# Performance work log

Measured on AMD Instinct MI355X. Metric: run time of the kernel, lower is better.

## Reference

```python
import jax, jax.numpy as jnp
import numpy as np

B, N1, N2, DIM1, DIM2, DK = 4, 4096, 2048, 256, 256, 256


def setup_inputs() -> dict:
    key = jax.random.key(0)
    ks = jax.random.split(key, 8)
    s1 = 1.0 / np.sqrt(DIM2)  # torch Linear default init scale (uniform bound)
    s2 = 1.0 / np.sqrt(DIM1)
    return {
        "x1": jax.random.normal(ks[0], (B, N1, DIM1), jnp.float32),
        "x2": jax.random.normal(ks[1], (B, N2, DIM2), jnp.float32),
        "WQ": jax.random.uniform(ks[2], (DK, DIM2), jnp.float32, -s1, s1),
        "bQ": jax.random.uniform(ks[3], (DK,), jnp.float32, -s1, s1),
        "WK": jax.random.uniform(ks[4], (DK, DIM1), jnp.float32, -s2, s2),
        "bK": jax.random.uniform(ks[5], (DK,), jnp.float32, -s2, s2),
        "WV": jax.random.uniform(ks[6], (DK, DIM1), jnp.float32, -s2, s2),
        "bV": jax.random.uniform(ks[7], (DK,), jnp.float32, -s2, s2),
    }


def reference(x1, x2, WQ, bQ, WK, bK, WV, bV):
    # Projections (torch Linear: x @ W^T + b)
    Q = jnp.einsum('bnd,kd->bnk', x2, WQ) + bQ  # [B, N2, DK]
    K = jnp.einsum('bmd,kd->bmk', x1, WK) + bK  # [B, N1, DK]
    V = jnp.einsum('bmd,kd->bmk', x1, WV) + bV  # [B, N1, DK]

    QK = jnp.einsum('bnk,bmk->bnm', Q, K)                          # [B, N2, N1]
    P = (jnp.einsum('bnk,bmk->bnm', jnp.tanh(Q), jnp.tanh(K)) + 1.0) * 0.5
    scores = QK * P / jnp.sqrt(jnp.float32(DK))
    attn = jax.nn.softmax(scores, axis=-1)                         # [B, N2, N1]
    Q_hat = jnp.einsum('bnm,bmk->bnk', attn, V)                    # [B, N2, DK]
    return (Q, Q_hat, attn)
```

## Files before the change

kernel.cpp:

```cpp
#include <hip/hip_runtime.h>
#include <hip/hip_bf16.h>

typedef __bf16 bf16;
typedef __bf16 bf16x4 __attribute__((ext_vector_type(4)));
typedef __bf16 bf16x8 __attribute__((ext_vector_type(8)));
typedef float  f32x4  __attribute__((ext_vector_type(4)));

#define DEVI static __device__ __forceinline__

constexpr int NB = 4;
constexpr int N1 = 4096;
constexpr int N2 = 2048;
constexpr int D  = 256;

DEVI f32x4 mfma16(bf16x8 a, bf16x8 b, f32x4 c) {
  return __builtin_amdgcn_mfma_f32_16x16x32_bf16(a, b, c, 0, 0, 0);
}

typedef const __attribute__((address_space(1))) void* gas_t;
typedef __attribute__((address_space(3))) void* las_t;

DEVI void gload_lds16(const void* g, void* l) {
  __builtin_amdgcn_global_load_lds((gas_t)g, (las_t)l, 16, 0, 0);
}

DEVI void fence_sched() { __builtin_amdgcn_sched_barrier(0); }

DEVI void projQ_body(bf16* smem,
                     const float* __restrict__ A, const float* __restrict__ Bm,
                     const float* __restrict__ bias,
                     float* __restrict__ outF, bf16* __restrict__ out1,
                     bf16* __restrict__ out2, int bx, int by)
{
  bf16* Ah = smem;
  bf16* Al = smem + 8192;
  bf16* Bh = smem + 16384;
  bf16* Bl = smem + 20480;
  const int tid  = threadIdx.x;
  const int lane = tid & 63, wid = tid >> 6;
  const int wr = wid >> 1, wc = wid & 1;
  const int m0 = bx * 128, n0 = by * 64;

  f32x4 acc[4][2];
#pragma unroll
  for (int i = 0; i < 4; ++i)
#pragma unroll
    for (int j = 0; j < 2; ++j) acc[i][j] = f32x4{0.f, 0.f, 0.f, 0.f};

  for (int kt = 0; kt < 4; ++kt) {
    const int k0 = kt * 64;
    if (kt) __syncthreads();
#pragma unroll
    for (int i = 0; i < 8; ++i) {
      int idx = i * 256 + tid;
      int r = idx >> 4, c4 = idx & 15;
      const float4 v = *(const float4*)(A + (size_t)(m0 + r) * D + k0 + c4 * 4);
      bf16x4 h, l;
      h[0] = (bf16)v.x; h[1] = (bf16)v.y; h[2] = (bf16)v.z; h[3] = (bf16)v.w;
      l[0] = (bf16)(v.x - (float)h[0]); l[1] = (bf16)(v.y - (float)h[1]);
      l[2] = (bf16)(v.z - (float)h[2]); l[3] = (bf16)(v.w - (float)h[3]);
      *(bf16x4*)&Ah[r * 64 + c4 * 4] = h;
      *(bf16x4*)&Al[r * 64 + c4 * 4] = l;
    }
#pragma unroll
    for (int i = 0; i < 4; ++i) {
      int idx = i * 256 + tid;
      int r = idx >> 4, c4 = idx & 15;
      const float4 v = *(const float4*)(Bm + (size_t)(n0 + r) * D + k0 + c4 * 4);
      bf16x4 h, l;
      h[0] = (bf16)v.x; h[1] = (bf16)v.y; h[2] = (bf16)v.z; h[3] = (bf16)v.w;
      l[0] = (bf16)(v.x - (float)h[0]); l[1] = (bf16)(v.y - (float)h[1]);
      l[2] = (bf16)(v.z - (float)h[2]); l[3] = (bf16)(v.w - (float)h[3]);
      *(bf16x4*)&Bh[r * 64 + c4 * 4] = h;
      *(bf16x4*)&Bl[r * 64 + c4 * 4] = l;
    }
    __syncthreads();
#pragma unroll
    for (int kc = 0; kc < 2; ++kc) {
      const int ko = kc * 32 + (lane >> 4) * 8;
      bf16x8 ah[4], al[4];
#pragma unroll
      for (int mf = 0; mf < 4; ++mf) {
        ah[mf] = *(bf16x8*)&Ah[(wr * 64 + mf * 16 + (lane & 15)) * 64 + ko];
        al[mf] = *(bf16x8*)&Al[(wr * 64 + mf * 16 + (lane & 15)) * 64 + ko];
      }
#pragma unroll
      for (int nf = 0; nf < 2; ++nf) {
        bf16x8 bh = *(bf16x8*)&Bh[(wc * 32 + nf * 16 + (lane & 15)) * 64 + ko];
        bf16x8 bl = *(bf16x8*)&Bl[(wc * 32 + nf * 16 + (lane & 15)) * 64 + ko];
#pragma unroll
        for (int mf = 0; mf < 4; ++mf) {
          acc[mf][nf] = mfma16(ah[mf], bh, acc[mf][nf]);
          acc[mf][nf] = mfma16(ah[mf], bl, acc[mf][nf]);
          acc[mf][nf] = mfma16(al[mf], bh, acc[mf][nf]);
        }
      }
    }
  }

#pragma unroll
  for (int nf = 0; nf < 2; ++nf) {
    const int col = n0 + wc * 32 + nf * 16 + (lane & 15);
    const float bcol = bias[col];
#pragma unroll
    for (int mf = 0; mf < 4; ++mf) {
#pragma unroll
      for (int r = 0; r < 4; ++r) {
        const int row = m0 + wr * 64 + mf * 16 + (lane >> 4) * 4 + r;
        float v = acc[mf][nf][r] + bcol;
        outF[(size_t)row * D + col] = v;
        out1[(size_t)row * D + col] = (bf16)v;
        out2[(size_t)row * D + col] = (bf16)tanhf(v);
      }
    }
  }
}

template<int MODE>
DEVI void proj_body(bf16* smem,
                    const float* __restrict__ A, const float* __restrict__ Bm,
                    const float* __restrict__ bias,
                    bf16* __restrict__ out1, bf16* __restrict__ out2,
                    int bx, int by)
{
  bf16* As = smem;
  bf16* Bs = smem + 8192;
  const int tid  = threadIdx.x;
  const int lane = tid & 63, wid = tid >> 6;
  const int wr = wid >> 1, wc = wid & 1;
  const int m0 = bx * 128, n0 = by * 64;

  f32x4 acc[4][2];
#pragma unroll
  for (int i = 0; i < 4; ++i)
#pragma unroll
    for (int j = 0; j < 2; ++j) acc[i][j] = f32x4{0.f, 0.f, 0.f, 0.f};

  for (int kt = 0; kt < 4; ++kt) {
    const int k0 = kt * 64;
    if (kt) __syncthreads();
#pragma unroll
    for (int i = 0; i < 8; ++i) {
      int idx = i * 256 + tid;
      int r = idx >> 4, c4 = idx & 15;
      const float4 v = *(const float4*)(A + (size_t)(m0 + r) * D + k0 + c4 * 4);
      bf16x4 bv; bv[0] = (bf16)v.x; bv[1] = (bf16)v.y; bv[2] = (bf16)v.z; bv[3] = (bf16)v.w;
      *(bf16x4*)&As[r * 64 + c4 * 4] = bv;
    }
#pragma unroll
    for (int i = 0; i < 4; ++i) {
      int idx = i * 256 + tid;
      int r = idx >> 4, c4 = idx & 15;
      const float4 v = *(const float4*)(Bm + (size_t)(n0 + r) * D + k0 + c4 * 4);
      bf16x4 bv; bv[0] = (bf16)v.x; bv[1] = (bf16)v.y; bv[2] = (bf16)v.z; bv[3] = (bf16)v.w;
      *(bf16x4*)&Bs[r * 64 + c4 * 4] = bv;
    }
    __syncthreads();
#pragma unroll
    for (int kc = 0; kc < 2; ++kc) {
      const int ko = kc * 32 + (lane >> 4) * 8;
      bf16x8 a[4];
#pragma unroll
      for (int mf = 0; mf < 4; ++mf)
        a[mf] = *(bf16x8*)&As[(wr * 64 + mf * 16 + (lane & 15)) * 64 + ko];
#pragma unroll
      for (int nf = 0; nf < 2; ++nf) {
        bf16x8 bb = *(bf16x8*)&Bs[(wc * 32 + nf * 16 + (lane & 15)) * 64 + ko];
#pragma unroll
        for (int mf = 0; mf < 4; ++mf) acc[mf][nf] = mfma16(a[mf], bb, acc[mf][nf]);
      }
    }
  }

#pragma unroll
  for (int nf = 0; nf < 2; ++nf) {
    const int col = n0 + wc * 32 + nf * 16 + (lane & 15);
    float bcol = 0.f;
    if constexpr (MODE == 1) bcol = bias[col];
#pragma unroll
    for (int mf = 0; mf < 4; ++mf) {
#pragma unroll
      for (int r = 0; r < 4; ++r) {
        const int row = m0 + wr * 64 + mf * 16 + (lane >> 4) * 4 + r;
        float v = acc[mf][nf][r];
        if constexpr (MODE == 1) {
          v += bcol;
          out1[(size_t)row * D + col] = (bf16)v;
          out2[(size_t)row * D + col] = (bf16)tanhf(v);
        } else {
          v += bias[row];
          out1[(size_t)(col >> 12) * (D * N1) + (size_t)row * N1 + (col & 4095)] = (bf16)v;
        }
      }
    }
  }
}

__global__ __launch_bounds__(256)
void proj_all_kernel(const float* __restrict__ x1, const float* __restrict__ x2,
                     const float* __restrict__ WQ, const float* __restrict__ bQ,
                     const float* __restrict__ WK, const float* __restrict__ bK,
                     const float* __restrict__ WV, const float* __restrict__ bV,
                     float* __restrict__ Qf, bf16* __restrict__ Qb,
                     bf16* __restrict__ tQb, bf16* __restrict__ Kb,
                     bf16* __restrict__ tKb, bf16* __restrict__ Vt)
{
  __shared__ bf16 smem[24576];
  const int bid = blockIdx.x;
  if (bid < 512) {
    proj_body<1>(smem, x1, WK, bK, Kb, tKb, bid & 127, bid >> 7);
  } else if (bid < 768) {
    const int b2 = bid - 512;
    projQ_body(smem, x2, WQ, bQ, Qf, Qb, tQb, b2 & 63, b2 >> 6);
  } else {
    const int b3 = bid - 768;
    proj_body<2>(smem, WV, x1, bV, Vt, nullptr, b3 & 1, b3 >> 1);
  }
}

__global__ __launch_bounds__(256, 2)
void scores_kernel(const bf16* __restrict__ Qb, const bf16* __restrict__ tQb,
                   const bf16* __restrict__ Kb, const bf16* __restrict__ tKb,
                   bf16* __restrict__ E, float* __restrict__ partials)
{
  __shared__ bf16 SM[2][4][128][32];
  __shared__ float rowpart[128][2];
  const int tid = threadIdx.x, lane = tid & 63, wid = tid >> 6;
  const int wr = wid >> 1;
  const int wc = wid & 1;
  const int lo16 = lane & 15, hi = lane >> 4;
  const int mt = blockIdx.x, nt = blockIdx.y, b = blockIdx.z;
  const int RQ = b * N2 + nt * 128;
  const int RK = b * N1 + mt * 128;

  f32x4 accS[4][4], accP[4][4];
#pragma unroll
  for (int i = 0; i < 4; ++i)
#pragma unroll
    for (int j = 0; j < 4; ++j) {
      accS[i][j] = f32x4{0.f, 0.f, 0.f, 0.f};
      accP[i][j] = f32x4{0.f, 0.f, 0.f, 0.f};
    }

  auto stage = [&](int kt, int buf) {
#pragma unroll
    for (int i = 0; i < 2; ++i) {
      const int c = i * 256 + tid;
      const int row = c >> 2;
      const int soff = kt * 32 + (((c & 3) ^ ((row >> 1) & 3)) << 3);
      char* dst = (char*)&SM[buf][0][0][0] + c * 16;
      gload_lds16(Qb  + (size_t)(RQ + row) * D + soff, dst);
      gload_lds16(tQb + (size_t)(RQ + row) * D + soff, dst + 8192);
      gload_lds16(Kb  + (size_t)(RK + row) * D + soff, dst + 16384);
      gload_lds16(tKb + (size_t)(RK + row) * D + soff, dst + 24576);
    }
  };

  auto cpt = [&](int buf) {
    bf16x8 aS[4], aT[4];
#pragma unroll
    for (int mf = 0; mf < 4; ++mf) {
      const int row = wr * 64 + mf * 16 + lo16;
      const int ko = (hi ^ ((row >> 1) & 3)) << 3;
      aS[mf] = *(bf16x8*)&SM[buf][0][row][ko];
      aT[mf] = *(bf16x8*)&SM[buf][1][row][ko];
    }
#pragma unroll
    for (int nf = 0; nf < 4; ++nf) {
      const int row = wc * 64 + nf * 16 + lo16;
      const int ko = (hi ^ ((row >> 1) & 3)) << 3;
      bf16x8 bS = *(bf16x8*)&SM[buf][2][row][ko];
      bf16x8 bT = *(bf16x8*)&SM[buf][3][row][ko];
#pragma unroll
      for (int mf = 0; mf < 4; ++mf) {
        accS[mf][nf] = mfma16(aS[mf], bS, accS[mf][nf]);
        accP[mf][nf] = mfma16(aT[mf], bT, accP[mf][nf]);
      }
    }
  };

  stage(0, 0);
  fence_sched();
  int cur = 0;
#pragma unroll
  for (int kt = 0; kt < 8; ++kt) {
    if (kt < 7) {
      stage(kt + 1, cur ^ 1);
      fence_sched();
      asm volatile("s_waitcnt vmcnt(8)\n\ts_barrier" ::: "memory");
    } else {
      asm volatile("s_waitcnt vmcnt(0)\n\ts_barrier" ::: "memory");
    }
    __builtin_amdgcn_s_setprio(1);
    cpt(cur);
    __builtin_amdgcn_s_setprio(0);
    asm volatile("s_barrier" ::: "memory");
    cur ^= 1;
  }

#pragma unroll
  for (int mf = 0; mf < 4; ++mf) {
    f32x4 rs = f32x4{0.f, 0.f, 0.f, 0.f};
#pragma unroll
    for (int nf = 0; nf < 4; ++nf) {
      const int m_g = mt * 128 + wc * 64 + nf * 16 + lo16;
#pragma unroll
      for (int r = 0; r < 4; ++r) {
        const int n_g = b * N2 + nt * 128 + wr * 64 + mf * 16 + hi * 4 + r;
        float s = accS[mf][nf][r] * (accP[mf][nf][r] + 1.0f) * 0.03125f;
        float e = __expf(s);
        E[(size_t)n_g * N1 + m_g] = (bf16)e;
        rs[r] += e;
      }
    }
#pragma unroll
    for (int r = 0; r < 4; ++r) {
      float v = rs[r];
      v += __shfl_xor(v, 1); v += __shfl_xor(v, 2);
      v += __shfl_xor(v, 4); v += __shfl_xor(v, 8);
      if (lo16 == 0)
        rowpart[wr * 64 + mf * 16 + hi * 4 + r][wc] = v;
    }
  }
  __syncthreads();
  if (tid < 128) {
    float p = rowpart[tid][0] + rowpart[tid][1];
    partials[(size_t)(b * N2 + nt * 128 + tid) * 32 + mt] = p;
  }
}

__global__ __launch_bounds__(512)
void qhat_kernel(const bf16* __restrict__ E, const bf16* __restrict__ Vt,
                 const float* __restrict__ partials,
                 float* __restrict__ attn, bf16* __restrict__ partQ)
{
  __shared__ bf16 Es[2][128][64];
  __shared__ bf16 Vs[2][256][64];
  __shared__ float rowinv[128];
  const int tid = threadIdx.x, lane = tid & 63, wid = tid >> 6;
  const int lo16 = lane & 15, hi = lane >> 4;
  const int wr = wid & 3;
  const int wh = wid >> 2;
  const int wgid = blockIdx.x;
  const int xcd  = wgid & 7;
  const int slot = wgid >> 3;
  const int combo = xcd * 2 + (slot >> 4);
  const int nt = slot & 15;
  const int q  = combo >> 2;
  const int b  = combo & 3;
  const int n0 = nt * 128;
  const int mq = q * 1024;
  const size_t nbase = (size_t)b * N2 + n0;
  const bf16* vb = Vt + (size_t)b * (D * N1) + mq;

  if (tid < 128) {
    const float* pr = partials + (nbase + tid) * 32;
    f32x4 s4 = *(const f32x4*)pr;
#pragma unroll
    for (int j = 1; j < 8; ++j) s4 += *(const f32x4*)(pr + j * 4);
    rowinv[tid] = 1.0f / (s4[0] + s4[1] + s4[2] + s4[3]);
  }

  auto stage = [&](int ms, int buf) {
#pragma unroll
    for (int i = 0; i < 2; ++i) {
      const int c = i * 512 + tid;
      const int row = c >> 3;
      const int lg = (c & 7) ^ (row & 7);
      gload_lds16(E + (nbase + row) * N1 + mq + ms * 64 + lg * 8,
                  (char*)&Es[buf][0][0] + c * 16);
    }
#pragma unroll
    for (int i = 0; i < 4; ++i) {
      const int c = i * 512 + tid;
      const int row = c >> 3;
      const int lg = (c & 7) ^ (row & 7);
      gload_lds16(vb + (size_t)row * N1 + ms * 64 + lg * 8,
                  (char*)&Vs[buf][0][0] + c * 16);
    }
  };

  f32x4 acc[2][8];
#pragma unroll
  for (int i = 0; i < 2; ++i)
#pragma unroll
    for (int j = 0; j < 8; ++j) acc[i][j] = f32x4{0.f, 0.f, 0.f, 0.f};

  auto cpt = [&](int buf) {
#pragma unroll
    for (int kc = 0; kc < 2; ++kc) {
      bf16x8 a[2];
#pragma unroll
      for (int mf = 0; mf < 2; ++mf) {
        const int row = wr * 32 + mf * 16 + lo16;
        const int ph = (kc * 4 + hi) ^ (row & 7);
        a[mf] = *(bf16x8*)((char*)&Es[buf][0][0] + row * 128 + ph * 16);
      }
#pragma unroll
      for (int nf = 0; nf < 8; ++nf) {
        const int row = wh * 128 + nf * 16 + lo16;
        const int ph = (kc * 4 + hi) ^ (row & 7);
        bf16x8 bb = *(bf16x8*)((char*)&Vs[buf][0][0] + row * 128 + ph * 16);
        acc[0][nf] = mfma16(a[0], bb, acc[0][nf]);
        acc[1][nf] = mfma16(a[1], bb, acc[1][nf]);
      }
    }
  };

  auto attnwrite = [&](int ms, int buf) {
#pragma unroll
    for (int i = 0; i < 2; ++i) {
      const int c = i * 512 + tid;
      const int row = c >> 3;
      const int lg = (c & 7) ^ (row & 7);
      bf16x8 ev = *(bf16x8*)((char*)&Es[buf][0][0] + c * 16);
      const float inv = rowinv[row];
      float v[8];
#pragma unroll
      for (int j = 0; j < 8; ++j) v[j] = (float)ev[j] * inv;
      float* dst = attn + (nbase + row) * N1 + mq + ms * 64 + lg * 8;
      float4 w0 = {v[0], v[1], v[2], v[3]};
      float4 w1 = {v[4], v[5], v[6], v[7]};
      *(float4*)(dst)     = w0;
      *(float4*)(dst + 4) = w1;
    }
  };

  stage(0, 0);
  fence_sched();
  __syncthreads();

  int buf = 0;
  for (int ms = 0; ms < 16; ++ms) {
    if (ms < 15) { stage(ms + 1, buf ^ 1); fence_sched(); }
    if (ms == 0)
      asm volatile("s_waitcnt vmcnt(6)\n\ts_barrier" ::: "memory");
    else if (ms < 15)
      asm volatile("s_waitcnt vmcnt(10)\n\ts_barrier" ::: "memory");
    else
      asm volatile("s_waitcnt vmcnt(4)\n\ts_barrier" ::: "memory");
    __builtin_amdgcn_s_setprio(1);
    cpt(buf);
    __builtin_amdgcn_s_setprio(0);
    attnwrite(ms, buf);
    asm volatile("s_barrier" ::: "memory");
    buf ^= 1;
  }

#pragma unroll
  for (int mf = 0; mf < 2; ++mf)
#pragma unroll
    for (int nf = 0; nf < 8; ++nf)
#pragma unroll
      for (int r = 0; r < 4; ++r) {
        const int n  = n0 + wr * 32 + mf * 16 + hi * 4 + r;
        const int dk = wh * 128 + nf * 16 + lo16;
        partQ[((size_t)(q * NB + b) * N2 + n) * D + dk] = (bf16)acc[mf][nf][r];
      }
}

__global__ __launch_bounds__(256)
void reduceQ_kernel(const bf16* __restrict__ P, const float* __restrict__ partials,
                    float* __restrict__ Qhat)
{
  const int tid = threadIdx.x;
  const size_t rn = (size_t)blockIdx.x * 8 + (tid >> 5);
  const int j = tid & 31;
  float s = partials[rn * 32 + j];
  s += __shfl_xor(s, 1); s += __shfl_xor(s, 2); s += __shfl_xor(s, 4);
  s += __shfl_xor(s, 8); s += __shfl_xor(s, 16);
  const float inv = 1.0f / s;

  const size_t base = rn * 256 + (size_t)j * 8;
  const size_t S = (size_t)NB * N2 * D;
  bf16x8 p0 = *(const bf16x8*)(P + base);
  bf16x8 p1 = *(const bf16x8*)(P + S + base);
  bf16x8 p2 = *(const bf16x8*)(P + 2 * S + base);
  bf16x8 p3 = *(const bf16x8*)(P + 3 * S + base);
  float o[8];
#pragma unroll
  for (int jj = 0; jj < 8; ++jj)
    o[jj] = (((float)p0[jj] + (float)p1[jj]) + ((float)p2[jj] + (float)p3[jj])) * inv;
  float4 w0 = {o[0], o[1], o[2], o[3]};
  float4 w1 = {o[4], o[5], o[6], o[7]};
  *(float4*)(Qhat + base)     = w0;
  *(float4*)(Qhat + base + 4) = w1;
}

extern "C" void kernel_launch(void* const* d_in, const int* in_sizes, int n_in,
                              void* d_out, int out_size, void* d_ws, size_t ws_size,
                              hipStream_t stream)
{
  const float* x1 = (const float*)d_in[0];
  const float* x2 = (const float*)d_in[1];
  const float* WQ = (const float*)d_in[2];
  const float* bQ = (const float*)d_in[3];
  const float* WK = (const float*)d_in[4];
  const float* bK = (const float*)d_in[5];
  const float* WV = (const float*)d_in[6];
  const float* bV = (const float*)d_in[7];

  float* out  = (float*)d_out;
  float* Qf   = out;
  float* Qhat = out + 2097152;
  float* attn = out + 4194304;

  char* ws = (char*)d_ws;
  bf16* Qb   = (bf16*)(ws + (0ull  << 20));
  bf16* tQb  = (bf16*)(ws + (4ull  << 20));
  bf16* Kb   = (bf16*)(ws + (8ull  << 20));
  bf16* tKb  = (bf16*)(ws + (16ull << 20));
  bf16* Vt   = (bf16*)(ws + (24ull << 20));
  bf16* E    = (bf16*)(ws + (32ull << 20));
  float* partials = (float*)(ws + (96ull << 20));
  bf16*  partQ    = (bf16*)(ws + (100ull << 20));

  proj_all_kernel <<<1280, 256, 0, stream>>>(x1, x2, WQ, bQ, WK, bK, WV, bV,
                                             Qf, Qb, tQb, Kb, tKb, Vt);
  scores_kernel   <<<dim3(32, 16, 4), 256, 0, stream>>>(Qb, tQb, Kb, tKb, E, partials);
  qhat_kernel     <<<256, 512, 0, stream>>>(E, Vt, partials, attn, partQ);
  reduceQ_kernel  <<<1024, 256, 0, stream>>>(partQ, partials, Qhat);
}
```

Before: 147.6 us.

## Widen scores tile to 128x256 with 8 waves and triple-buffered K-loop

The scores kernel now computes a 128x256 output tile per block using 512 threads (8 waves in a 2x4 grid), so each staged Q tile is reused across twice as many K rows. This halves the number of blocks and the Q reload traffic. The K-loop moves from double to triple buffering with a prefetch distance of two and adjusted vmcnt waits, to hide more global-load latency. Per-row partial sums drop from 32 to 16 entries, and the downstream qhat and reduce kernels are updated to match. Shared memory per block grows and occupancy falls to one large block per CU.

```diff
diff --git a/kernel.cpp b/kernel.cpp
--- a/kernel.cpp
+++ b/kernel.cpp
@@ -218,20 +218,21 @@
   }
 }
 
-__global__ __launch_bounds__(256, 2)
+__global__ __launch_bounds__(512, 1)
 void scores_kernel(const bf16* __restrict__ Qb, const bf16* __restrict__ tQb,
                    const bf16* __restrict__ Kb, const bf16* __restrict__ tKb,
                    bf16* __restrict__ E, float* __restrict__ partials)
 {
-  __shared__ bf16 SM[2][4][128][32];
-  __shared__ float rowpart[128][2];
+  __shared__ bf16 SMQ[3][2][128][32];
+  __shared__ bf16 SMK[3][2][256][32];
+  __shared__ float rowpart[128][4];
   const int tid = threadIdx.x, lane = tid & 63, wid = tid >> 6;
-  const int wr = wid >> 1;
-  const int wc = wid & 1;
+  const int wr = wid >> 2;
+  const int wc = wid & 3;
   const int lo16 = lane & 15, hi = lane >> 4;
   const int mt = blockIdx.x, nt = blockIdx.y, b = blockIdx.z;
   const int RQ = b * N2 + nt * 128;
-  const int RK = b * N1 + mt * 128;
+  const int RK = b * N1 + mt * 256;
 
   f32x4 accS[4][4], accP[4][4];
 #pragma unroll
@@ -242,17 +243,24 @@
       accP[i][j] = f32x4{0.f, 0.f, 0.f, 0.f};
     }
 
+  const int qrow = tid >> 2;
+  const int qsc  = (((tid & 3) ^ ((qrow >> 1) & 3)) << 3);
+
   auto stage = [&](int kt, int buf) {
+    const int k0 = kt * 32;
+    gload_lds16(Qb  + (size_t)(RQ + qrow) * D + k0 + qsc,
+                (char*)&SMQ[buf][0][0][0] + tid * 16);
+    gload_lds16(tQb + (size_t)(RQ + qrow) * D + k0 + qsc,
+                (char*)&SMQ[buf][1][0][0] + tid * 16);
 #pragma unroll
     for (int i = 0; i < 2; ++i) {
-      const int c = i * 256 + tid;
+      const int c = i * 512 + tid;
       const int row = c >> 2;
-      const int soff = kt * 32 + (((c & 3) ^ ((row >> 1) & 3)) << 3);
-      char* dst = (char*)&SM[buf][0][0][0] + c * 16;
-      gload_lds16(Qb  + (size_t)(RQ + row) * D + soff, dst);
-      gload_lds16(tQb + (size_t)(RQ + row) * D + soff, dst + 8192);
-      gload_lds16(Kb  + (size_t)(RK + row) * D + soff, dst + 16384);
-      gload_lds16(tKb + (size_t)(RK + row) * D + soff, dst + 24576);
+      const int sc = (((c & 3) ^ ((row >> 1) & 3)) << 3);
+      gload_lds16(Kb  + (size_t)(RK + row) * D + k0 + sc,
+                  (char*)&SMK[buf][0][0][0] + c * 16);
+      gload_lds16(tKb + (size_t)(RK + row) * D + k0 + sc,
+                  (char*)&SMK[buf][1][0][0] + c * 16);
     }
   };
 
@@ -262,15 +270,15 @@
     for (int mf = 0; mf < 4; ++mf) {
       const int row = wr * 64 + mf * 16 + lo16;
       const int ko = (hi ^ ((row >> 1) & 3)) << 3;
-      aS[mf] = *(bf16x8*)&SM[buf][0][row][ko];
-      aT[mf] = *(bf16x8*)&SM[buf][1][row][ko];
+      aS[mf] = *(bf16x8*)&SMQ[buf][0][row][ko];
+      aT[mf] = *(bf16x8*)&SMQ[buf][1][row][ko];
     }
 #pragma unroll
     for (int nf = 0; nf < 4; ++nf) {
       const int row = wc * 64 + nf * 16 + lo16;
       const int ko = (hi ^ ((row >> 1) & 3)) << 3;
-      bf16x8 bS = *(bf16x8*)&SM[buf][2][row][ko];
-      bf16x8 bT = *(bf16x8*)&SM[buf][3][row][ko];
+      bf16x8 bS = *(bf16x8*)&SMK[buf][0][row][ko];
+      bf16x8 bT = *(bf16x8*)&SMK[buf][1][row][ko];
 #pragma unroll
       for (int mf = 0; mf < 4; ++mf) {
         accS[mf][nf] = mfma16(aS[mf], bS, accS[mf][nf]);
@@ -281,21 +289,26 @@
 
   stage(0, 0);
   fence_sched();
-  int cur = 0;
+  stage(1, 1);
+  fence_sched();
 #pragma unroll
   for (int kt = 0; kt < 8; ++kt) {
-    if (kt < 7) {
-      stage(kt + 1, cur ^ 1);
+    const int buf = kt - (kt / 3) * 3;
+    if (kt < 6) {
+      const int nb = (kt + 2) - ((kt + 2) / 3) * 3;
+      stage(kt + 2, nb);
       fence_sched();
-      asm volatile("s_waitcnt vmcnt(8)\n\ts_barrier" ::: "memory");
-    } else {
+    }
+    if (kt < 6)
+      asm volatile("s_waitcnt vmcnt(12)\n\ts_barrier" ::: "memory");
+    else if (kt == 6)
+      asm volatile("s_waitcnt vmcnt(6)\n\ts_barrier" ::: "memory");
+    else
       asm volatile("s_waitcnt vmcnt(0)\n\ts_barrier" ::: "memory");
-    }
     __builtin_amdgcn_s_setprio(1);
-    cpt(cur);
+    cpt(buf);
     __builtin_amdgcn_s_setprio(0);
     asm volatile("s_barrier" ::: "memory");
-    cur ^= 1;
   }
 
 #pragma unroll
@@ -303,7 +316,7 @@
     f32x4 rs = f32x4{0.f, 0.f, 0.f, 0.f};
 #pragma unroll
     for (int nf = 0; nf < 4; ++nf) {
-      const int m_g = mt * 128 + wc * 64 + nf * 16 + lo16;
+      const int m_g = mt * 256 + wc * 64 + nf * 16 + lo16;
 #pragma unroll
       for (int r = 0; r < 4; ++r) {
         const int n_g = b * N2 + nt * 128 + wr * 64 + mf * 16 + hi * 4 + r;
@@ -324,8 +337,8 @@
   }
   __syncthreads();
   if (tid < 128) {
-    float p = rowpart[tid][0] + rowpart[tid][1];
-    partials[(size_t)(b * N2 + nt * 128 + tid) * 32 + mt] = p;
+    float p = rowpart[tid][0] + rowpart[tid][1] + rowpart[tid][2] + rowpart[tid][3];
+    partials[(size_t)(b * N2 + nt * 128 + tid) * 16 + mt] = p;
   }
 }
 
@@ -354,10 +367,10 @@
   const bf16* vb = Vt + (size_t)b * (D * N1) + mq;
 
   if (tid < 128) {
-    const float* pr = partials + (nbase + tid) * 32;
+    const float* pr = partials + (nbase + tid) * 16;
     f32x4 s4 = *(const f32x4*)pr;
 #pragma unroll
-    for (int j = 1; j < 8; ++j) s4 += *(const f32x4*)(pr + j * 4);
+    for (int j = 1; j < 4; ++j) s4 += *(const f32x4*)(pr + j * 4);
     rowinv[tid] = 1.0f / (s4[0] + s4[1] + s4[2] + s4[3]);
   }
 
@@ -466,9 +479,9 @@
   const int tid = threadIdx.x;
   const size_t rn = (size_t)blockIdx.x * 8 + (tid >> 5);
   const int j = tid & 31;
-  float s = partials[rn * 32 + j];
+  float s = partials[rn * 16 + (j & 15)];
   s += __shfl_xor(s, 1); s += __shfl_xor(s, 2); s += __shfl_xor(s, 4);
-  s += __shfl_xor(s, 8); s += __shfl_xor(s, 16);
+  s += __shfl_xor(s, 8);
   const float inv = 1.0f / s;
 
   const size_t base = rn * 256 + (size_t)j * 8;
@@ -517,7 +530,7 @@
 
   proj_all_kernel <<<1280, 256, 0, stream>>>(x1, x2, WQ, bQ, WK, bK, WV, bV,
                                              Qf, Qb, tQb, Kb, tKb, Vt);
-  scores_kernel   <<<dim3(32, 16, 4), 256, 0, stream>>>(Qb, tQb, Kb, tKb, E, partials);
+  scores_kernel   <<<dim3(16, 16, 4), 512, 0, stream>>>(Qb, tQb, Kb, tKb, E, partials);
   qhat_kernel     <<<256, 512, 0, stream>>>(E, Vt, partials, attn, partQ);
   reduceQ_kernel  <<<1024, 256, 0, stream>>>(partQ, partials, Qhat);
 }
```

New measurement: 149.3 us. Within noise of the previous version (+1.1%).

## Fuse Q-hat split reduction into qhat kernel via last-block atomic counter

Applied to the files above, without the earlier changes.

Removes the separate reduceQ kernel launch. Each qhat workgroup now atomically increments a per-(batch,row-tile) counter after writing its partial Q-hat, and the last of the four split-M workgroups sums the partials and normalizes them using the already-loaded row inverse. The counters are zeroed in the projection kernel. This saves a launch and a pass over the partials, but the reduction tail now runs serially inside the last-arriving workgroups and adds fences and atomics.

```diff
diff --git a/kernel.cpp b/kernel.cpp
--- a/kernel.cpp
+++ b/kernel.cpp
@@ -203,10 +203,12 @@
                      const float* __restrict__ WV, const float* __restrict__ bV,
                      float* __restrict__ Qf, bf16* __restrict__ Qb,
                      bf16* __restrict__ tQb, bf16* __restrict__ Kb,
-                     bf16* __restrict__ tKb, bf16* __restrict__ Vt)
+                     bf16* __restrict__ tKb, bf16* __restrict__ Vt,
+                     int* __restrict__ qcnt)
 {
   __shared__ bf16 smem[24576];
   const int bid = blockIdx.x;
+  if (bid == 0 && threadIdx.x < 64) qcnt[threadIdx.x] = 0;
   if (bid < 512) {
     proj_body<1>(smem, x1, WK, bK, Kb, tKb, bid & 127, bid >> 7);
   } else if (bid < 768) {
@@ -332,11 +334,13 @@
 __global__ __launch_bounds__(512)
 void qhat_kernel(const bf16* __restrict__ E, const bf16* __restrict__ Vt,
                  const float* __restrict__ partials,
-                 float* __restrict__ attn, bf16* __restrict__ partQ)
+                 float* __restrict__ attn, bf16* __restrict__ partQ,
+                 float* __restrict__ Qhat, int* __restrict__ qcnt)
 {
   __shared__ bf16 Es[2][128][64];
   __shared__ bf16 Vs[2][256][64];
   __shared__ float rowinv[128];
+  __shared__ int lastflag;
   const int tid = threadIdx.x, lane = tid & 63, wid = tid >> 6;
   const int lo16 = lane & 15, hi = lane >> 4;
   const int wr = wid & 3;
@@ -457,34 +461,39 @@
         const int dk = wh * 128 + nf * 16 + lo16;
         partQ[((size_t)(q * NB + b) * N2 + n) * D + dk] = (bf16)acc[mf][nf][r];
       }
-}
-
-__global__ __launch_bounds__(256)
-void reduceQ_kernel(const bf16* __restrict__ P, const float* __restrict__ partials,
-                    float* __restrict__ Qhat)
-{
-  const int tid = threadIdx.x;
-  const size_t rn = (size_t)blockIdx.x * 8 + (tid >> 5);
-  const int j = tid & 31;
-  float s = partials[rn * 32 + j];
-  s += __shfl_xor(s, 1); s += __shfl_xor(s, 2); s += __shfl_xor(s, 4);
-  s += __shfl_xor(s, 8); s += __shfl_xor(s, 16);
-  const float inv = 1.0f / s;
-
-  const size_t base = rn * 256 + (size_t)j * 8;
-  const size_t S = (size_t)NB * N2 * D;
-  bf16x8 p0 = *(const bf16x8*)(P + base);
-  bf16x8 p1 = *(const bf16x8*)(P + S + base);
-  bf16x8 p2 = *(const bf16x8*)(P + 2 * S + base);
-  bf16x8 p3 = *(const bf16x8*)(P + 3 * S + base);
-  float o[8];
-#pragma unroll
-  for (int jj = 0; jj < 8; ++jj)
-    o[jj] = (((float)p0[jj] + (float)p1[jj]) + ((float)p2[jj] + (float)p3[jj])) * inv;
-  float4 w0 = {o[0], o[1], o[2], o[3]};
-  float4 w1 = {o[4], o[5], o[6], o[7]};
-  *(float4*)(Qhat + base)     = w0;
-  *(float4*)(Qhat + base + 4) = w1;
+
+  __threadfence();
+  __syncthreads();
+  if (tid == 0) {
+    int old = atomicAdd(&qcnt[b * 16 + nt], 1);
+    lastflag = (old == 3);
+  }
+  __syncthreads();
+  if (lastflag) {
+    __threadfence();
+    const size_t S = (size_t)NB * N2 * D;
+    const size_t gbase = ((size_t)b * N2 + n0) * D;
+#pragma unroll
+    for (int i = 0; i < 8; ++i) {
+      const int item = i * 512 + tid;
+      const int row = item >> 5;
+      const int ch  = item & 31;
+      const size_t off = gbase + (size_t)row * D + ch * 8;
+      bf16x8 p0 = *(const bf16x8*)(partQ + off);
+      bf16x8 p1 = *(const bf16x8*)(partQ + S + off);
+      bf16x8 p2 = *(const bf16x8*)(partQ + 2 * S + off);
+      bf16x8 p3 = *(const bf16x8*)(partQ + 3 * S + off);
+      const float inv = rowinv[row];
+      float o[8];
+#pragma unroll
+      for (int jj = 0; jj < 8; ++jj)
+        o[jj] = (((float)p0[jj] + (float)p1[jj]) + ((float)p2[jj] + (float)p3[jj])) * inv;
+      float4 w0 = {o[0], o[1], o[2], o[3]};
+      float4 w1 = {o[4], o[5], o[6], o[7]};
+      *(float4*)(Qhat + off)     = w0;
+      *(float4*)(Qhat + off + 4) = w1;
+    }
+  }
 }
 
 extern "C" void kernel_launch(void* const* d_in, const int* in_sizes, int n_in,
@@ -513,11 +522,11 @@
   bf16* Vt   = (bf16*)(ws + (24ull << 20));
   bf16* E    = (bf16*)(ws + (32ull << 20));
   float* partials = (float*)(ws + (96ull << 20));
+  int*   qcnt     = (int*)(ws + (99ull << 20));
   bf16*  partQ    = (bf16*)(ws + (100ull << 20));
 
   proj_all_kernel <<<1280, 256, 0, stream>>>(x1, x2, WQ, bQ, WK, bK, WV, bV,
-                                             Qf, Qb, tQb, Kb, tKb, Vt);
+                                             Qf, Qb, tQb, Kb, tKb, Vt, qcnt);
   scores_kernel   <<<dim3(32, 16, 4), 256, 0, stream>>>(Qb, tQb, Kb, tKb, E, partials);
-  qhat_kernel     <<<256, 512, 0, stream>>>(E, Vt, partials, attn, partQ);
-  reduceQ_kernel  <<<1024, 256, 0, stream>>>(partQ, partials, Qhat);
-}
+  qhat_kernel     <<<256, 512, 0, stream>>>(E, Vt, partials, attn, partQ, Qhat, qcnt);
+}
```

Result: slower. 254.9 us (+72.7%).
